# Performance work log

Measured on AMD Instinct MI355X. Metric: run time of the kernel, lower is better.

## Reference

```python
import jax, jax.numpy as jnp
import numpy as np

DIM, HEADS = 768, 12


def setup_inputs() -> dict:
    key = jax.random.key(0)
    ks = jax.random.split(key, 9)
    B, N, C, H = 4, 1024, DIM, HEADS
    s = 0.02
    return {
        "x": jax.random.normal(ks[0], (B, N, C), jnp.float32),
        "W_qkv": jax.random.normal(ks[1], (C, 3 * C), jnp.float32) * s,
        "W_proj": jax.random.normal(ks[2], (C, C), jnp.float32) * s,
        "b_proj": jax.random.normal(ks[3], (C,), jnp.float32) * s,
        "W_l": jax.random.normal(ks[4], (H, H), jnp.float32) * s,
        "b_l": jax.random.normal(ks[5], (H,), jnp.float32) * s,
        "W_w": jax.random.normal(ks[6], (H, H), jnp.float32) * s,
        "b_w": jax.random.normal(ks[7], (H,), jnp.float32) * s,
        "lamb": jax.random.normal(ks[8], (H,), jnp.float32) * 0.1,
    }


def reference(x, W_qkv, W_proj, b_proj, W_l, b_l, W_w, b_w, lamb):
    B, N, C = x.shape
    H = W_l.shape[0]
    d = C // H
    scale = d ** -0.5

    qkv = (x @ W_qkv).reshape(B, N, 3, H, d)  # [B,N,3,H,d]
    q = qkv[:, :, 0].transpose(0, 2, 1, 3) * scale  # [B,H,N,d]
    k = qkv[:, :, 1].transpose(0, 2, 1, 3)
    v = qkv[:, :, 2].transpose(0, 2, 1, 3)

    attn = jnp.einsum("bhnd,bhmd->bhnm", q, k)  # [B,H,N,N]
    # talking-heads mix before softmax (proj_l over head axis)
    attn = jnp.einsum("bhnm,hg->bgnm", attn, W_l) + b_l[None, :, None, None]
    attn = jax.nn.softmax(attn, axis=-1)
    # talking-heads mix after softmax (proj_w)
    attn = jnp.einsum("bhnm,hg->bgnm", attn, W_w) + b_w[None, :, None, None]

    # attnscale reaction term: (h-1)*(attn - I)@attn + attn, h=4
    eye = jnp.eye(N, dtype=attn.dtype)
    reaction = 3.0 * jnp.einsum("bhnk,bhkm->bhnm", attn - eye, attn) + attn
    attn = attn + lamb[None, :, None, None] * reaction

    out = jnp.einsum("bhnm,bhmd->bhnd", attn, v)  # [B,H,N,d]
    out = out.transpose(0, 2, 1, 3).reshape(B, N, C)
    return out @ W_proj + b_proj
```

## Files before the change

### kernel.cpp

```cpp
#include <hip/hip_runtime.h>
#include <hip/hip_bf16.h>
#include <stdint.h>

#define B_ 4
#define N_ 1024
#define C_ 768
#define H_ 12
#define D_ 64

typedef unsigned short u16;
typedef __attribute__((ext_vector_type(8))) short bf16x8;
typedef __attribute__((ext_vector_type(4))) float f32x4;

#define AS1 __attribute__((address_space(1)))
#define AS3 __attribute__((address_space(3)))

__device__ __forceinline__ u16 f2b(float f) {
    union { float f; uint32_t u; } x; x.f = f;
    uint32_t r = x.u + 0x7fffu + ((x.u >> 16) & 1u);
    return (u16)(r >> 16);
}
__device__ __forceinline__ float b2f(u16 b) {
    union { uint32_t u; float f; } x; x.u = ((uint32_t)b) << 16;
    return x.f;
}
__device__ __forceinline__ uint32_t cvtpk(float lo, float hi) {
    uint32_t r;
    asm("v_cvt_pk_bf16_f32 %0, %1, %2" : "=v"(r) : "v"(lo), "v"(hi));
    return r;
}

__device__ __forceinline__ void gload16(const void* g, void* lds) {
    __builtin_amdgcn_global_load_lds((const AS1 uint32_t*)g, (AS3 uint32_t*)lds, 16, 0, 0);
}

__device__ __forceinline__ void stage_tile(const u16* __restrict__ g, int ld,
                                           u16* lds, int rows, int w, int l) {
    int nchunk = rows >> 3;
    for (int j = w; j < nchunk; j += 4) {
        int base = j << 10;
        int lanebyte = base + (l << 4);
        int row  = lanebyte >> 7;
        int slot = ((lanebyte >> 4) & 7) ^ (row & 7);
        const u16* src = g + row * ld + (slot << 3);
        gload16(src, (char*)lds + base);
    }
}

__device__ __forceinline__ bf16x8 frag_ld(const u16* lds, int row, int k) {
    int byte = (row << 7) + (k << 1);
    byte ^= (row & 7) << 4;
    return *(const bf16x8*)((const char*)lds + byte);
}

__device__ __forceinline__ f32x4 mfma_bf16(bf16x8 a, bf16x8 b, f32x4 c) {
    return __builtin_amdgcn_mfma_f32_16x16x32_bf16(a, b, c, 0, 0, 0);
}


__global__ void k_cvt(const float* __restrict__ in, u16* __restrict__ outb) {
    int i = blockIdx.x * blockDim.x + threadIdx.x;
    float4 v = ((const float4*)in)[i];
    ushort4 o;
    o.x = f2b(v.x); o.y = f2b(v.y); o.z = f2b(v.z); o.w = f2b(v.w);
    ((ushort4*)outb)[i] = o;
}

__global__ void k_transcvt(const float* __restrict__ in, u16* __restrict__ outb,
                           int R, int Cc) {
    __shared__ float t[32][33];
    int bc = blockIdx.x * 32, br = blockIdx.y * 32;
    int tid = threadIdx.x;
    for (int i = 0; i < 4; i++) {
        int idx = i * 256 + tid; int r = idx >> 5, c = idx & 31;
        t[r][c] = in[(size_t)(br + r) * Cc + bc + c];
    }
    __syncthreads();
    for (int i = 0; i < 4; i++) {
        int idx = i * 256 + tid; int c = idx >> 5, r = idx & 31;
        outb[(size_t)(bc + c) * R + br + r] = f2b(t[r][c]);
    }
}

__global__ void k_vT(const u16* __restrict__ qkv, u16* __restrict__ vT) {
    __shared__ u16 t[64][72];
    int blk = blockIdx.x;
    int nt = blk & 15, h = (blk >> 4) % H_, b = blk / (H_ * 16);
    int tid = threadIdx.x;
    const u16* src = qkv + ((size_t)(b * N_ + nt * 64)) * (3 * C_) + 2 * C_ + h * 64;
    for (int i = 0; i < 16; i++) {
        int idx = i * 256 + tid; int n = idx >> 6, dd = idx & 63;
        t[n][dd] = src[(size_t)n * (3 * C_) + dd];
    }
    __syncthreads();
    u16* dst = vT + ((size_t)(b * H_ + h) * D_) * N_ + nt * 64;
    for (int i = 0; i < 16; i++) {
        int idx = i * 256 + tid; int dd = idx >> 6, n = idx & 63;
        dst[(size_t)dd * N_ + n] = t[n][dd];
    }
}


__global__ __launch_bounds__(256, 2)
void k_gemm_qkv(const u16* __restrict__ xb, const u16* __restrict__ WT,
                u16* __restrict__ qkv) {
    __shared__ __attribute__((aligned(128))) u16 As[128 * 64];
    __shared__ __attribute__((aligned(128))) u16 Bs[128 * 64];
    int tid = threadIdx.x, w = tid >> 6, l = tid & 63;
    int row0 = blockIdx.x * 128, col0 = blockIdx.y * 128;
    f32x4 acc[4][4] = {};
    int wr = (w >> 1) * 64, wc = (w & 1) * 64;
    int fr = l & 15, fq = l >> 4;
    for (int k0 = 0; k0 < C_; k0 += 64) {
        stage_tile(xb + (size_t)row0 * C_ + k0, C_, As, 128, w, l);
        stage_tile(WT + (size_t)col0 * C_ + k0, C_, Bs, 128, w, l);
        __syncthreads();
        #pragma unroll
        for (int kk = 0; kk < 64; kk += 32) {
            bf16x8 af[4], bfr[4];
            #pragma unroll
            for (int i = 0; i < 4; i++) af[i] = frag_ld(As, wr + i * 16 + fr, kk + fq * 8);
            #pragma unroll
            for (int j = 0; j < 4; j++) bfr[j] = frag_ld(Bs, wc + j * 16 + fr, kk + fq * 8);
            #pragma unroll
            for (int i = 0; i < 4; i++)
                #pragma unroll
                for (int j = 0; j < 4; j++)
                    acc[i][j] = mfma_bf16(af[i], bfr[j], acc[i][j]);
        }
        __syncthreads();
    }
    #pragma unroll
    for (int i = 0; i < 4; i++) {
        #pragma unroll
        for (int j = 0; j < 4; j++) {
            int col = col0 + wc + j * 16 + fr;
            float s = (col < C_) ? 0.125f : 1.0f;
            #pragma unroll
            for (int r = 0; r < 4; r++) {
                int row = row0 + wr + i * 16 + fq * 4 + r;
                qkv[(size_t)row * (3 * C_) + col] = f2b(acc[i][j][r] * s);
            }
        }
    }
}


__global__ __launch_bounds__(256, 2)
void k_gemm_qk(const u16* __restrict__ qkv, u16* __restrict__ S) {
    __shared__ __attribute__((aligned(128))) u16 pool[128 * 132];
    u16* As = pool;
    u16* Bs = pool + 128 * 64;
    int tid = threadIdx.x, w = tid >> 6, l = tid & 63;
    int blk = blockIdx.x;
    int bh = blk >> 6, t = blk & 63;
    int b = bh / H_, h = bh % H_;
    int tm = t >> 3, tn = t & 7;
    const u16* qbase = qkv + (size_t)(b * N_) * (3 * C_) + h * 64;
    const u16* kbase = qkv + (size_t)(b * N_) * (3 * C_) + C_ + h * 64;
    f32x4 acc[4][4] = {};
    int wr = (w >> 1) * 64, wc = (w & 1) * 64;
    int fr = l & 15, fq = l >> 4;
    stage_tile(qbase + (size_t)(tm * 128) * (3 * C_), 3 * C_, As, 128, w, l);
    stage_tile(kbase + (size_t)(tn * 128) * (3 * C_), 3 * C_, Bs, 128, w, l);
    __syncthreads();
    #pragma unroll
    for (int kk = 0; kk < 64; kk += 32) {
        bf16x8 af[4], bfr[4];
        #pragma unroll
        for (int i = 0; i < 4; i++) af[i] = frag_ld(As, wr + i * 16 + fr, kk + fq * 8);
        #pragma unroll
        for (int j = 0; j < 4; j++) bfr[j] = frag_ld(Bs, wc + j * 16 + fr, kk + fq * 8);
        #pragma unroll
        for (int i = 0; i < 4; i++)
            #pragma unroll
            for (int j = 0; j < 4; j++)
                acc[i][j] = mfma_bf16(af[i], bfr[j], acc[i][j]);
    }
    __syncthreads();
    u16* Cs = pool;
    #pragma unroll
    for (int i = 0; i < 4; i++) {
        #pragma unroll
        for (int j = 0; j < 4; j++) {
            int lcol = wc + j * 16 + fr;
            #pragma unroll
            for (int r = 0; r < 4; r++) {
                int lrow = wr + i * 16 + fq * 4 + r;
                Cs[lrow * 132 + lcol] = f2b(acc[i][j][r]);
            }
        }
    }
    __syncthreads();
    for (int q = 0; q < 16; q++) {
        int idx = q * 256 + tid;
        int lrow = idx >> 5, lc = idx & 31;
        ushort4 v = *(const ushort4*)&Cs[lrow * 132 + lc * 4];
        *(ushort4*)(S + ((size_t)(b * N_ + tm * 128 + lrow) * H_ + h) * N_
                      + tn * 128 + lc * 4) = v;
    }
}


__global__ __launch_bounds__(256)
void k_mix_softmax(const u16* __restrict__ S, u16* __restrict__ Pw,
                   const float* __restrict__ Wl, const float* __restrict__ Ww,
                   const float* __restrict__ bw) {
    __shared__ __attribute__((aligned(16))) u16 Sb[4][2][256][8];
    __shared__ float Zl[4][16];
    __shared__ float sWl[144], sWw[144], sbw16[16];
    int tid = threadIdx.x;
    int wv = tid >> 6, l = tid & 63;
    int m_l = l & 15, gr = l >> 4;
    if (tid < 144) { sWl[tid] = Wl[tid]; sWw[tid] = Ww[tid]; }
    if (tid < 16) sbw16[tid] = (tid < 12) ? bw[tid] : 0.f;
    __syncthreads();

    int blk = blockIdx.x;
    int b = blk >> 10, n = blk & 1023;
    const u16* srow = S + ((size_t)(b * N_ + n) * H_) * N_ + wv * 256;

    for (int p = 0; p < 4; p++) {
        int m = p * 64 + l;
        #pragma unroll
        for (int hb = 0; hb < 2; hb++) {
            bf16x8 pk;
            #pragma unroll
            for (int j = 0; j < 8; j++) {
                int h = hb * 8 + j;
                ((u16*)&pk)[j] = (h < 12) ? srow[(size_t)h * N_ + m] : (u16)0;
            }
            *(bf16x8*)&Sb[wv][hb][m][0] = pk;
        }
    }

    bf16x8 a1;
    #pragma unroll
    for (int j = 0; j < 8; j++) {
        int h = gr * 8 + j;
        int ok = (m_l < 12) & (h < 12);
        int idx = ok ? (h * 12 + m_l) : 0;
        float wval = ok ? sWl[idx] : 0.f;
        ((u16*)&a1)[j] = f2b(wval);
    }

    float z0 = 0.f, z1 = 0.f, z2 = 0.f, z3 = 0.f;
    uint32_t E0[16], E1[16];
    #pragma unroll
    for (int grp = 0; grp < 16; grp++) {
        bf16x8 bs = {};
        if (gr < 2) bs = *(const bf16x8*)&Sb[wv][gr][grp * 16 + m_l][0];
        f32x4 c = {0.f, 0.f, 0.f, 0.f};
        c = mfma_bf16(a1, bs, c);
        float e0 = __expf(c[0]), e1 = __expf(c[1]);
        float e2 = __expf(c[2]), e3 = __expf(c[3]);
        z0 += e0; z1 += e1; z2 += e2; z3 += e3;
        E0[grp] = cvtpk(e0, e1);
        E1[grp] = cvtpk(e2, e3);
    }

    #pragma unroll
    for (int off = 1; off < 16; off <<= 1) {
        z0 += __shfl_xor(z0, off);
        z1 += __shfl_xor(z1, off);
        z2 += __shfl_xor(z2, off);
        z3 += __shfl_xor(z3, off);
    }
    if (m_l == 0) {
        Zl[wv][gr * 4 + 0] = z0; Zl[wv][gr * 4 + 1] = z1;
        Zl[wv][gr * 4 + 2] = z2; Zl[wv][gr * 4 + 3] = z3;
    }
    __syncthreads();

    bf16x8 a2;
    #pragma unroll
    for (int j = 0; j < 8; j++) {
        int h = gr * 8 + j;
        float v = 0.f;
        if ((m_l < 12) & (h < 12)) {
            float zz = Zl[0][h] + Zl[1][h] + Zl[2][h] + Zl[3][h];
            v = sWw[h * 12 + m_l] / zz;
        }
        ((u16*)&a2)[j] = f2b(v);
    }

    f32x4 cb;
    cb[0] = sbw16[gr * 4 + 0]; cb[1] = sbw16[gr * 4 + 1];
    cb[2] = sbw16[gr * 4 + 2]; cb[3] = sbw16[gr * 4 + 3];
    int la = m_l + (((2 * gr) & 3) << 4);
    int lb = m_l + (((2 * gr + 1) & 3) << 4);
    u16* Pb = (u16*)&Sb[wv][0][0][0];
    #pragma unroll
    for (int grp = 0; grp < 16; grp++) {
        union { int4 i4; bf16x8 v; } u;
        u.i4.x = __shfl((int)E0[grp], la);
        u.i4.y = __shfl((int)E1[grp], la);
        u.i4.z = __shfl((int)E0[grp], lb);
        u.i4.w = __shfl((int)E1[grp], lb);
        f32x4 c = cb;
        c = mfma_bf16(a2, u.v, c);
        if (gr < 3) {
            uint32_t w01 = cvtpk(c[0], c[1]);
            uint32_t w23 = cvtpk(c[2], c[3]);
            int g0 = gr * 4, mm = grp * 16 + m_l;
            Pb[(g0 + 0) * 276 + mm] = (u16)w01;
            Pb[(g0 + 1) * 276 + mm] = (u16)(w01 >> 16);
            Pb[(g0 + 2) * 276 + mm] = (u16)w23;
            Pb[(g0 + 3) * 276 + mm] = (u16)(w23 >> 16);
        }
    }

    for (int g = 0; g < 12; g++) {
        ushort4 v = *(const ushort4*)&Pb[g * 276 + l * 4];
        *(ushort4*)(Pw + ((size_t)(b * H_ + g) * N_ + n) * N_ + wv * 256 + l * 4) = v;
    }
}


template <int MODE>
__global__ __launch_bounds__(256, 2)
void k_gemm_av(const u16* __restrict__ Pw, const u16* __restrict__ BT,
               u16* __restrict__ outp, const float* __restrict__ lamb) {
    __shared__ __attribute__((aligned(128))) u16 As[64 * 64];
    __shared__ __attribute__((aligned(128))) u16 Bs[64 * 64];
    int tid = threadIdx.x, w = tid >> 6, l = tid & 63;
    int blk = blockIdx.x;
    int bh = blk >> 4, tm = blk & 15;
    int b = bh / H_, h = bh % H_;
    const u16* Abase = Pw + ((size_t)bh * N_ + tm * 64) * N_;
    const u16* Bbase = BT + (size_t)bh * D_ * N_;
    f32x4 acc[4] = {};
    int wrow = w * 16;
    int fr = l & 15, fq = l >> 4;
    for (int k0 = 0; k0 < N_; k0 += 64) {
        stage_tile(Abase + k0, N_, As, 64, w, l);
        stage_tile(Bbase + k0, N_, Bs, 64, w, l);
        __syncthreads();
        #pragma unroll
        for (int kk = 0; kk < 64; kk += 32) {
            bf16x8 af = frag_ld(As, wrow + fr, kk + fq * 8);
            bf16x8 bfr[4];
            #pragma unroll
            for (int j = 0; j < 4; j++) bfr[j] = frag_ld(Bs, j * 16 + fr, kk + fq * 8);
            #pragma unroll
            for (int j = 0; j < 4; j++)
                acc[j] = mfma_bf16(af, bfr[j], acc[j]);
        }
        __syncthreads();
    }
    float lam = (MODE == 0) ? lamb[h] : 0.f;
    #pragma unroll
    for (int j = 0; j < 4; j++) {
        int col = j * 16 + fr;
        int rowb = tm * 64 + wrow + fq * 4;
        if (MODE == 0) {
            ushort4 vv = *(const ushort4*)(BT + ((size_t)bh * D_ + col) * N_ + rowb);
            ushort4 zo;
            #pragma unroll
            for (int r = 0; r < 4; r++) {
                float zv = (1.f - 2.f * lam) * b2f(((const u16*)&vv)[r])
                         + 3.f * lam * acc[j][r];
                ((u16*)&zo)[r] = f2b(zv);
            }
            *(ushort4*)(outp + ((size_t)bh * D_ + col) * N_ + rowb) = zo;
        } else {
            #pragma unroll
            for (int r = 0; r < 4; r++)
                outp[(size_t)(b * N_ + rowb + r) * C_ + h * 64 + col] = f2b(acc[j][r]);
        }
    }
}


__global__ __launch_bounds__(256, 2)
void k_gemm_proj(const u16* __restrict__ o, const u16* __restrict__ WT,
                 const float* __restrict__ bias, float* __restrict__ out) {
    __shared__ __attribute__((aligned(128))) u16 As[128 * 64];
    __shared__ __attribute__((aligned(128))) u16 Bs[128 * 64];
    int tid = threadIdx.x, w = tid >> 6, l = tid & 63;
    int row0 = blockIdx.x * 128, col0 = blockIdx.y * 128;
    f32x4 acc[4][4] = {};
    int wr = (w >> 1) * 64, wc = (w & 1) * 64;
    int fr = l & 15, fq = l >> 4;
    for (int k0 = 0; k0 < C_; k0 += 64) {
        stage_tile(o + (size_t)row0 * C_ + k0, C_, As, 128, w, l);
        stage_tile(WT + (size_t)col0 * C_ + k0, C_, Bs, 128, w, l);
        __syncthreads();
        #pragma unroll
        for (int kk = 0; kk < 64; kk += 32) {
            bf16x8 af[4], bfr[4];
            #pragma unroll
            for (int i = 0; i < 4; i++) af[i] = frag_ld(As, wr + i * 16 + fr, kk + fq * 8);
            #pragma unroll
            for (int j = 0; j < 4; j++) bfr[j] = frag_ld(Bs, wc + j * 16 + fr, kk + fq * 8);
            #pragma unroll
            for (int i = 0; i < 4; i++)
                #pragma unroll
                for (int j = 0; j < 4; j++)
                    acc[i][j] = mfma_bf16(af[i], bfr[j], acc[i][j]);
        }
        __syncthreads();
    }
    #pragma unroll
    for (int i = 0; i < 4; i++) {
        #pragma unroll
        for (int j = 0; j < 4; j++) {
            int col = col0 + wc + j * 16 + fr;
            float bv = bias[col];
            #pragma unroll
            for (int r = 0; r < 4; r++) {
                int row = row0 + wr + i * 16 + fq * 4 + r;
                out[(size_t)row * C_ + col] = acc[i][j][r] + bv;
            }
        }
    }
}


extern "C" void kernel_launch(void* const* d_in, const int* in_sizes, int n_in,
                              void* d_out, int out_size, void* d_ws, size_t ws_size,
                              hipStream_t stream) {
    const float* x     = (const float*)d_in[0];
    const float* Wqkv  = (const float*)d_in[1];
    const float* Wproj = (const float*)d_in[2];
    const float* bproj = (const float*)d_in[3];
    const float* Wl    = (const float*)d_in[4];
    const float* Ww    = (const float*)d_in[6];
    const float* bw    = (const float*)d_in[7];
    const float* lamb  = (const float*)d_in[8];
    float* out = (float*)d_out;
    char* ws = (char*)d_ws;

    constexpr size_t SZ_S   = (size_t)B_ * N_ * H_ * N_ * 2;
    constexpr size_t SZ_QKV = (size_t)B_ * N_ * 3 * C_ * 2;
    constexpr size_t SZ_U   = (size_t)B_ * H_ * N_ * D_ * 2;
    constexpr size_t SZ_XB  = (size_t)B_ * N_ * C_ * 2;
    constexpr size_t SZ_WQT = (size_t)C_ * 3 * C_ * 2;

    u16* S      = (u16*)(ws);
    u16* zT     = (u16*)(ws);
    u16* o      = (u16*)(ws + SZ_U);
    u16* Pw     = (u16*)(ws + SZ_S);
    u16* qkv    = (u16*)(ws + 2 * SZ_S);
    u16* xb     = (u16*)(ws + 2 * SZ_S + SZ_QKV);
    u16* vT     = xb;
    u16* WqkvT  = (u16*)(ws + 2 * SZ_S + SZ_QKV + SZ_XB);
    u16* WprojT = (u16*)(ws + 2 * SZ_S + SZ_QKV + SZ_XB + SZ_WQT);

    k_cvt<<<3072, 256, 0, stream>>>(x, xb);
    k_transcvt<<<dim3(72, 24), 256, 0, stream>>>(Wqkv, WqkvT, C_, 3 * C_);
    k_transcvt<<<dim3(24, 24), 256, 0, stream>>>(Wproj, WprojT, C_, C_);
    k_gemm_qkv<<<dim3(32, 18), 256, 0, stream>>>(xb, WqkvT, qkv);
    k_vT<<<B_ * H_ * 16, 256, 0, stream>>>(qkv, vT);
    k_gemm_qk<<<B_ * H_ * 64, 256, 0, stream>>>(qkv, S);
    k_mix_softmax<<<B_ * N_, 256, 0, stream>>>(S, Pw, Wl, Ww, bw);
    k_gemm_av<0><<<B_ * H_ * 16, 256, 0, stream>>>(Pw, vT, zT, lamb);
    k_gemm_av<1><<<B_ * H_ * 16, 256, 0, stream>>>(Pw, zT, o, nullptr);
    k_gemm_proj<<<dim3(32, 6), 256, 0, stream>>>(o, WprojT, bproj, out);
}
```

Before: 176.8 us.

## Merge prep kernels, vectorize softmax S loads with swizzled LDS, use exp2

Folds the x conversion and the two weight transpose-conversions into a single k_prep launch, removing two kernel launches. In the mix-softmax kernel, each lane now loads 4 contiguous bf16 per head as uint2 and repacks them with byte permutes into a swizzled LDS layout, replacing 16-bit scalar gathers. The exp is switched to exp2 by folding log2(e) into the W_l mixing weights. The wider loads cut global load instruction count, and the XOR swizzle is meant to reduce LDS bank conflicts. The cost is extra permute arithmetic, slightly different rounding from the bf16 weight scaling, and softmax still runs without max subtraction.

```diff
diff --git a/kernel.cpp b/kernel.cpp
--- a/kernel.cpp
+++ b/kernel.cpp
@@ -58,19 +58,29 @@
 }
 
 
-__global__ void k_cvt(const float* __restrict__ in, u16* __restrict__ outb) {
-    int i = blockIdx.x * blockDim.x + threadIdx.x;
-    float4 v = ((const float4*)in)[i];
-    ushort4 o;
-    o.x = f2b(v.x); o.y = f2b(v.y); o.z = f2b(v.z); o.w = f2b(v.w);
-    ((ushort4*)outb)[i] = o;
-}
-
-__global__ void k_transcvt(const float* __restrict__ in, u16* __restrict__ outb,
-                           int R, int Cc) {
+__global__ void k_prep(const float* __restrict__ x, u16* __restrict__ xb,
+                       const float* __restrict__ Wqkv, u16* __restrict__ WqkvT,
+                       const float* __restrict__ Wproj, u16* __restrict__ WprojT) {
     __shared__ float t[32][33];
-    int bc = blockIdx.x * 32, br = blockIdx.y * 32;
+    int blk = blockIdx.x;
     int tid = threadIdx.x;
+    if (blk < 3072) {
+        int i = blk * 256 + tid;
+        float4 v = ((const float4*)x)[i];
+        ushort4 o;
+        o.x = f2b(v.x); o.y = f2b(v.y); o.z = f2b(v.z); o.w = f2b(v.w);
+        ((ushort4*)xb)[i] = o;
+        return;
+    }
+    const float* in; u16* outb; int R, Cc, bx, by;
+    if (blk < 3072 + 1728) {
+        int tq = blk - 3072;
+        in = Wqkv; outb = WqkvT; R = C_; Cc = 3 * C_; bx = tq % 72; by = tq / 72;
+    } else {
+        int tq = blk - 4800;
+        in = Wproj; outb = WprojT; R = C_; Cc = C_; bx = tq % 24; by = tq / 24;
+    }
+    int bc = bx * 32, br = by * 32;
     for (int i = 0; i < 4; i++) {
         int idx = i * 256 + tid; int r = idx >> 5, c = idx & 31;
         t[r][c] = in[(size_t)(br + r) * Cc + bc + c];
@@ -219,19 +229,33 @@
     int blk = blockIdx.x;
     int b = blk >> 10, n = blk & 1023;
     const u16* srow = S + ((size_t)(b * N_ + n) * H_) * N_ + wv * 256;
-
-    for (int p = 0; p < 4; p++) {
-        int m = p * 64 + l;
-        #pragma unroll
-        for (int hb = 0; hb < 2; hb++) {
-            bf16x8 pk;
-            #pragma unroll
-            for (int j = 0; j < 8; j++) {
-                int h = hb * 8 + j;
-                ((u16*)&pk)[j] = (h < 12) ? srow[(size_t)h * N_ + m] : (u16)0;
-            }
-            *(bf16x8*)&Sb[wv][hb][m][0] = pk;
-        }
+    char* sbase = (char*)&Sb[wv][0][0][0];
+
+    uint2 Hq[12];
+    #pragma unroll
+    for (int h = 0; h < 12; h++)
+        Hq[h] = *(const uint2*)(srow + (size_t)h * N_ + 4 * l);
+    #pragma unroll
+    for (int r = 0; r < 4; r++) {
+        int m = 4 * l + r;
+        int mp = m ^ ((m >> 3) & 3);
+        uint32_t sel = (r & 1) ? 0x07060302u : 0x05040100u;
+        union { uint32_t d[4]; bf16x8 v; } p0, p1;
+        #pragma unroll
+        for (int k = 0; k < 4; k++) {
+            uint32_t lo = (r < 2) ? Hq[2 * k].x     : Hq[2 * k].y;
+            uint32_t hi = (r < 2) ? Hq[2 * k + 1].x : Hq[2 * k + 1].y;
+            p0.d[k] = __builtin_amdgcn_perm(hi, lo, sel);
+        }
+        #pragma unroll
+        for (int k = 0; k < 2; k++) {
+            uint32_t lo = (r < 2) ? Hq[8 + 2 * k].x     : Hq[8 + 2 * k].y;
+            uint32_t hi = (r < 2) ? Hq[8 + 2 * k + 1].x : Hq[8 + 2 * k + 1].y;
+            p1.d[k] = __builtin_amdgcn_perm(hi, lo, sel);
+        }
+        p1.d[2] = 0; p1.d[3] = 0;
+        *(bf16x8*)(sbase + mp * 16)        = p0.v;
+        *(bf16x8*)(sbase + 4096 + mp * 16) = p1.v;
     }
 
     bf16x8 a1;
@@ -240,7 +264,7 @@
         int h = gr * 8 + j;
         int ok = (m_l < 12) & (h < 12);
         int idx = ok ? (h * 12 + m_l) : 0;
-        float wval = ok ? sWl[idx] : 0.f;
+        float wval = ok ? (sWl[idx] * 1.44269504089f) : 0.f;
         ((u16*)&a1)[j] = f2b(wval);
     }
 
@@ -249,11 +273,15 @@
     #pragma unroll
     for (int grp = 0; grp < 16; grp++) {
         bf16x8 bs = {};
-        if (gr < 2) bs = *(const bf16x8*)&Sb[wv][gr][grp * 16 + m_l][0];
+        if (gr < 2) {
+            int m = grp * 16 + m_l;
+            int mp = m ^ ((m >> 3) & 3);
+            bs = *(const bf16x8*)(sbase + gr * 4096 + mp * 16);
+        }
         f32x4 c = {0.f, 0.f, 0.f, 0.f};
         c = mfma_bf16(a1, bs, c);
-        float e0 = __expf(c[0]), e1 = __expf(c[1]);
-        float e2 = __expf(c[2]), e3 = __expf(c[3]);
+        float e0 = exp2f(c[0]), e1 = exp2f(c[1]);
+        float e2 = exp2f(c[2]), e3 = exp2f(c[3]);
         z0 += e0; z1 += e1; z2 += e2; z3 += e3;
         E0[grp] = cvtpk(e0, e1);
         E1[grp] = cvtpk(e2, e3);
@@ -447,9 +475,7 @@
     u16* WqkvT  = (u16*)(ws + 2 * SZ_S + SZ_QKV + SZ_XB);
     u16* WprojT = (u16*)(ws + 2 * SZ_S + SZ_QKV + SZ_XB + SZ_WQT);
 
-    k_cvt<<<3072, 256, 0, stream>>>(x, xb);
-    k_transcvt<<<dim3(72, 24), 256, 0, stream>>>(Wqkv, WqkvT, C_, 3 * C_);
-    k_transcvt<<<dim3(24, 24), 256, 0, stream>>>(Wproj, WprojT, C_, C_);
+    k_prep<<<5376, 256, 0, stream>>>(x, xb, Wqkv, WqkvT, Wproj, WprojT);
     k_gemm_qkv<<<dim3(32, 18), 256, 0, stream>>>(xb, WqkvT, qkv);
     k_vT<<<B_ * H_ * 16, 256, 0, stream>>>(qkv, vT);
     k_gemm_qk<<<B_ * H_ * 64, 256, 0, stream>>>(qkv, S);
```

Result: no change. 176.8 us (-0.0%).
